# Kernel tuning notes

Measured on AMD Instinct MI355X. Metric: run time of the kernel, lower is better.

## Reference

```python
import jax, jax.numpy as jnp
import numpy as np

OBS_LEN = 16          # observation_len in SnapKV
KERNEL = 5            # AvgPool1d kernel_size
MAX_CACHE_LEN = 2048  # max_cache_length


def _avg_pool1d_nopad(x, k=KERNEL):
    """AvgPool1d(kernel=k, stride=1, padding=k//2, count_include_pad=False) over last axis."""
    S = x.shape[-1]
    pad = k // 2
    zero = jnp.zeros(x.shape[:-1] + (1,), x.dtype)
    c0 = jnp.concatenate([zero, jnp.cumsum(x, axis=-1)], axis=-1)  # [..., S+1]
    i = jnp.arange(S)
    hi = jnp.minimum(i + pad + 1, S)  # exclusive window end
    lo = jnp.maximum(i - pad, 0)      # inclusive window start
    wsum = jnp.take(c0, hi, axis=-1) - jnp.take(c0, lo, axis=-1)
    return wsum / (hi - lo).astype(x.dtype)


def setup_inputs() -> dict:
    key = jax.random.key(0)
    k1, k2, k3 = jax.random.split(key, 3)
    B, H, Q, S, D = 1, 32, 64, 8192, 128
    # realistic attention weights: softmax over key axis
    attn = jax.nn.softmax(jax.random.normal(k1, (B, H, Q, S), jnp.float32), axis=-1)
    k_val = jax.random.normal(k2, (B, H, S, D), jnp.float32)
    v_val = jax.random.normal(k3, (B, H, S, D), jnp.float32)
    input_pos = jnp.arange(S, dtype=jnp.int32)
    return {"attn": attn, "k_val": k_val, "v_val": v_val, "input_pos": input_pos}


def reference(attn, k_val, v_val, input_pos):
    # ---- SnapKV prompt compression (_compress_prompt_w_snapkv) ----
    # priority: mean attention received by each key over the last OBS_LEN queries
    priority = attn[:, :, -OBS_LEN:, :].mean(axis=2)          # [B, H, S]
    attn_history = priority                                    # pre-pooling copy
    pooled = _avg_pool1d_nopad(priority)                       # [B, H, S]
    pooled = pooled.at[:, :, -OBS_LEN:].set(1.0)               # always keep observation window
    _, keep_idxs = jax.lax.top_k(pooled, MAX_CACHE_LEN)        # [B, H, L]
    keep_idxs = jnp.sort(keep_idxs, axis=-1)
    attn_history_c = jnp.take_along_axis(attn_history, keep_idxs, axis=-1)  # [B, H, L]
    idx4 = keep_idxs[..., None]                                # [B, H, L, 1]
    k_compressed = jnp.take_along_axis(k_val, idx4, axis=2)    # [B, H, L, D]
    v_compressed = jnp.take_along_axis(v_val, idx4, axis=2)    # [B, H, L, D]
    # ---- cache fill (update / fill_headwise): compressed tokens fill the whole cache ----
    k_cache = k_compressed
    v_cache = v_compressed
    pos = keep_idxs[0].astype(jnp.int32)                       # head-specific positions, [H, L]
    return k_cache, v_cache, attn_history_c, pos
```

## Files before the change

### kernel.cpp

```cpp
#include <hip/hip_runtime.h>

#define H 32
#define Q 64
#define S 8192
#define D 128
#define OBS 16
#define L 2048

__global__ void k_priority(const float* __restrict__ attn, float* __restrict__ prio) {
    int gid = blockIdx.x;
    int h = gid >> 3;
    int chunk = gid & 7;
    int s4 = chunk * 1024 + threadIdx.x * 4;
    const float4* base = (const float4*)(attn + ((size_t)(h * Q + (Q - OBS)) * S + s4));
    float4 acc = make_float4(0.f, 0.f, 0.f, 0.f);
#pragma unroll
    for (int qq = 0; qq < OBS; ++qq) {
        float4 v = base[qq * (S / 4)];
        acc.x += v.x; acc.y += v.y; acc.z += v.z; acc.w += v.w;
    }
    const float inv = 1.0f / (float)OBS;
    acc.x *= inv; acc.y *= inv; acc.z *= inv; acc.w *= inv;
    *((float4*)(prio + (size_t)h * S + s4)) = acc;
}

__global__ __launch_bounds__(1024) void k_select(const float* __restrict__ prio,
                                                 int* __restrict__ keep,
                                                 float* __restrict__ hist_out,
                                                 float* __restrict__ pos_out) {
    __shared__ float pr[S];
    __shared__ int whist[16][257];
    __shared__ int wtot[16];
    __shared__ int res_byte, res_k;
    const int h = blockIdx.x;
    const int tid = threadIdx.x;
    const int lane = tid & 63, wid = tid >> 6;

    {
        const float4* src = (const float4*)(prio + (size_t)h * S);
        ((float4*)pr)[tid] = src[tid];
        ((float4*)pr)[tid + 1024] = src[tid + 1024];
    }
    __syncthreads();

    unsigned key[8];
    const int s0 = tid * 8;
    {
        float w[12];
#pragma unroll
        for (int i = 0; i < 12; ++i) {
            int idx = s0 - 2 + i;
            w[i] = (idx >= 0 && idx < S) ? pr[idx] : 0.f;
        }
#pragma unroll
        for (int j = 0; j < 8; ++j) {
            int s = s0 + j;
            float pooled;
            if (s >= S - OBS) {
                pooled = 1.0f;
            } else {
                int lo = s - 2; if (lo < 0) lo = 0;
                int hi = s + 3;
                float sum = 0.f;
                for (int i = lo; i < hi; ++i) sum += w[i - s0 + 2];
                pooled = sum / (float)(hi - lo);
            }
            key[j] = __float_as_uint(pooled);
        }
    }

    unsigned prefix = 0;
    int k = L;
    for (int pass = 3; pass >= 0; --pass) {
        for (int i = tid; i < 16 * 257; i += 1024) ((int*)whist)[i] = 0;
        __syncthreads();
        const int shift = pass * 8;
        {
            int cur = -1, run = 0;
#pragma unroll
            for (int j = 0; j < 8; ++j) {
                unsigned kk = key[j];
                bool match = (pass == 3) || ((kk >> (shift + 8)) == prefix);
                int b = match ? (int)((kk >> shift) & 255u) : -1;
                if (b != cur) {
                    if (cur >= 0) atomicAdd(&whist[wid][cur], run);
                    cur = b; run = 1;
                } else {
                    run++;
                }
            }
            if (cur >= 0) atomicAdd(&whist[wid][cur], run);
        }
        __syncthreads();
        if (wid == 0) {
            int b0 = 0, b1 = 0, b2 = 0, b3 = 0;
            const int bb0 = 4 * lane;
#pragma unroll
            for (int w = 0; w < 16; ++w) {
                b0 += whist[w][bb0 + 0];
                b1 += whist[w][bb0 + 1];
                b2 += whist[w][bb0 + 2];
                b3 += whist[w][bb0 + 3];
            }
            int lane_sum = b0 + b1 + b2 + b3;
            int suffix = lane_sum;
#pragma unroll
            for (int off = 1; off < 64; off <<= 1) {
                int u = __shfl_down(suffix, off);
                if (lane + off < 64) suffix += u;
            }
            int suffix_next = suffix - lane_sum;
            if (suffix >= k && suffix_next < k) {
                int bins[4] = {b0, b1, b2, b3};
                int cum = suffix_next;
                for (int bb = 3; bb >= 0; --bb) {
                    int nc = cum + bins[bb];
                    if (nc >= k) { res_byte = bb0 + bb; res_k = k - cum; break; }
                    cum = nc;
                }
            }
        }
        __syncthreads();
        prefix = (prefix << 8) | (unsigned)res_byte;
        k = res_k;
    }
    const unsigned T = prefix;
    const int needed_eq = k;

    int gt = 0, eq = 0;
#pragma unroll
    for (int j = 0; j < 8; ++j) {
        gt += (key[j] > T) ? 1 : 0;
        eq += (key[j] == T) ? 1 : 0;
    }
    int packed = (gt << 16) | eq;
    int v = packed;
#pragma unroll
    for (int off = 1; off < 64; off <<= 1) {
        int u = __shfl_up(v, off);
        if (lane >= off) v += u;
    }
    if (lane == 63) wtot[wid] = v;
    __syncthreads();
    int base = 0;
    for (int w = 0; w < wid; ++w) base += wtot[w];
    int excl = base + v - packed;
    int gt_before = excl >> 16;
    int eq_before = excl & 0xffff;

    {
        int g = gt_before, e = eq_before;
#pragma unroll
        for (int j = 0; j < 8; ++j) {
            bool isgt = key[j] > T;
            bool iseq = key[j] == T;
            bool sel = isgt || (iseq && (e < needed_eq));
            if (sel) {
                int s = s0 + j;
                int rank = g + (e < needed_eq ? e : needed_eq);
                size_t o = (size_t)h * L + rank;
                keep[o] = s;
                pos_out[o] = (float)s;
                hist_out[o] = pr[s];
            }
            g += isgt ? 1 : 0;
            e += iseq ? 1 : 0;
        }
    }
}

__global__ void k_gather(const float* __restrict__ kv_k, const float* __restrict__ kv_v,
                         const int* __restrict__ keep, float* __restrict__ out) {
    const int tid = threadIdx.x;
    const int idx = blockIdx.x * 8 + (tid >> 5);
    const int lane = tid & 31;
    const int h = idx >> 11;
    const int s = keep[idx];
    const float4* srcK = (const float4*)(kv_k + (size_t)(h * S + s) * D);
    const float4* srcV = (const float4*)(kv_v + (size_t)(h * S + s) * D);
    float4* dstK = (float4*)(out + (size_t)idx * D);
    float4* dstV = (float4*)(out + ((size_t)H * L + idx) * D);
    dstK[lane] = srcK[lane];
    dstV[lane] = srcV[lane];
}

extern "C" void kernel_launch(void* const* d_in, const int* in_sizes, int n_in,
                              void* d_out, int out_size, void* d_ws, size_t ws_size,
                              hipStream_t stream) {
    const float* attn = (const float*)d_in[0];
    const float* k_val = (const float*)d_in[1];
    const float* v_val = (const float*)d_in[2];

    float* out = (float*)d_out;
    float* hist = out + (size_t)2 * H * L * D;
    float* pos = hist + (size_t)H * L;

    float* prio = (float*)d_ws;
    int* keep = (int*)((char*)d_ws + (size_t)H * S * sizeof(float));

    k_priority<<<256, 256, 0, stream>>>(attn, prio);
    k_select<<<H, 1024, 0, stream>>>(prio, keep, hist, pos);
    k_gather<<<(H * L) / 8, 256, 0, stream>>>(k_val, v_val, keep, out);
}
```

Measured before the change: 296.9 us.

## Fuse priority, selection and gather into one persistent kernel with flag sync

Merges the three kernels into a single 256-block launch. Every block computes one priority chunk, the first 32 blocks then run the per-head radix select, and all blocks gather K/V rows once their head's selection flag is set. Global-memory counters and flags, reset by a memset, replace the kernel boundaries. This removes launch gaps and lets the gather for finished heads overlap with selection of others, but it relies on all 256 blocks being co-resident (spin-waits could deadlock otherwise) and adds a memset launch.

```diff
diff --git a/kernel.cpp b/kernel.cpp
--- a/kernel.cpp
+++ b/kernel.cpp
@@ -7,181 +7,216 @@
 #define OBS 16
 #define L 2048
 
-__global__ void k_priority(const float* __restrict__ attn, float* __restrict__ prio) {
-    int gid = blockIdx.x;
-    int h = gid >> 3;
-    int chunk = gid & 7;
-    int s4 = chunk * 1024 + threadIdx.x * 4;
-    const float4* base = (const float4*)(attn + ((size_t)(h * Q + (Q - OBS)) * S + s4));
-    float4 acc = make_float4(0.f, 0.f, 0.f, 0.f);
-#pragma unroll
-    for (int qq = 0; qq < OBS; ++qq) {
-        float4 v = base[qq * (S / 4)];
-        acc.x += v.x; acc.y += v.y; acc.z += v.z; acc.w += v.w;
-    }
-    const float inv = 1.0f / (float)OBS;
-    acc.x *= inv; acc.y *= inv; acc.z *= inv; acc.w *= inv;
-    *((float4*)(prio + (size_t)h * S + s4)) = acc;
-}
-
-__global__ __launch_bounds__(1024) void k_select(const float* __restrict__ prio,
-                                                 int* __restrict__ keep,
-                                                 float* __restrict__ hist_out,
-                                                 float* __restrict__ pos_out) {
+__global__ __launch_bounds__(1024) void k_fused(
+    const float* __restrict__ attn,
+    const float* __restrict__ kv_k,
+    const float* __restrict__ kv_v,
+    float* __restrict__ prio,
+    int* __restrict__ keep,
+    int* __restrict__ pdone,
+    int* __restrict__ sflag,
+    float* __restrict__ out,
+    float* __restrict__ hist_out,
+    float* __restrict__ pos_out)
+{
     __shared__ float pr[S];
     __shared__ int whist[16][257];
     __shared__ int wtot[16];
     __shared__ int res_byte, res_k;
-    const int h = blockIdx.x;
+
+    const int bid = blockIdx.x;
     const int tid = threadIdx.x;
     const int lane = tid & 63, wid = tid >> 6;
 
+    if (tid < 256) {
+        const int h = bid >> 3;
+        const int chunk = bid & 7;
+        const int s4 = chunk * 1024 + tid * 4;
+        const float4* base = (const float4*)(attn + ((size_t)(h * Q + (Q - OBS)) * S + s4));
+        float4 acc = make_float4(0.f, 0.f, 0.f, 0.f);
+#pragma unroll
+        for (int qq = 0; qq < OBS; ++qq) {
+            float4 v = base[qq * (S / 4)];
+            acc.x += v.x; acc.y += v.y; acc.z += v.z; acc.w += v.w;
+        }
+        const float inv = 1.0f / (float)OBS;
+        acc.x *= inv; acc.y *= inv; acc.z *= inv; acc.w *= inv;
+        *((float4*)(prio + (size_t)(bid >> 3) * S + s4)) = acc;
+    }
+    __syncthreads();
+    if (tid == 0) {
+        __threadfence();
+        atomicAdd(&pdone[bid >> 3], 1);
+    }
+
+    if (bid < H) {
+        const int h = bid;
+        if (tid == 0) {
+            while (atomicAdd(&pdone[h], 0) < 8) __builtin_amdgcn_s_sleep(2);
+            __threadfence();
+        }
+        __syncthreads();
+
+        {
+            const float4* src = (const float4*)(prio + (size_t)h * S);
+            ((float4*)pr)[tid] = src[tid];
+            ((float4*)pr)[tid + 1024] = src[tid + 1024];
+        }
+        __syncthreads();
+
+        unsigned key[8];
+        const int s0 = tid * 8;
+        {
+            float w[12];
+#pragma unroll
+            for (int i = 0; i < 12; ++i) {
+                int idx = s0 - 2 + i;
+                w[i] = (idx >= 0 && idx < S) ? pr[idx] : 0.f;
+            }
+#pragma unroll
+            for (int j = 0; j < 8; ++j) {
+                int s = s0 + j;
+                float pooled;
+                if (s >= S - OBS) {
+                    pooled = 1.0f;
+                } else {
+                    int lo = s - 2; if (lo < 0) lo = 0;
+                    int hi = s + 3;
+                    float sum = 0.f;
+                    for (int i = lo; i < hi; ++i) sum += w[i - s0 + 2];
+                    pooled = sum / (float)(hi - lo);
+                }
+                key[j] = __float_as_uint(pooled);
+            }
+        }
+
+        unsigned prefix = 0;
+        int k = L;
+        for (int pass = 3; pass >= 0; --pass) {
+            for (int i = tid; i < 16 * 257; i += 1024) ((int*)whist)[i] = 0;
+            __syncthreads();
+            const int shift = pass * 8;
+            {
+                int cur = -1, run = 0;
+#pragma unroll
+                for (int j = 0; j < 8; ++j) {
+                    unsigned kk = key[j];
+                    bool match = (pass == 3) || ((kk >> (shift + 8)) == prefix);
+                    int b = match ? (int)((kk >> shift) & 255u) : -1;
+                    if (b != cur) {
+                        if (cur >= 0) atomicAdd(&whist[wid][cur], run);
+                        cur = b; run = 1;
+                    } else {
+                        run++;
+                    }
+                }
+                if (cur >= 0) atomicAdd(&whist[wid][cur], run);
+            }
+            __syncthreads();
+            if (wid == 0) {
+                int b0 = 0, b1 = 0, b2 = 0, b3 = 0;
+                const int bb0 = 4 * lane;
+#pragma unroll
+                for (int w = 0; w < 16; ++w) {
+                    b0 += whist[w][bb0 + 0];
+                    b1 += whist[w][bb0 + 1];
+                    b2 += whist[w][bb0 + 2];
+                    b3 += whist[w][bb0 + 3];
+                }
+                int lane_sum = b0 + b1 + b2 + b3;
+                int suffix = lane_sum;
+#pragma unroll
+                for (int off = 1; off < 64; off <<= 1) {
+                    int u = __shfl_down(suffix, off);
+                    if (lane + off < 64) suffix += u;
+                }
+                int suffix_next = suffix - lane_sum;
+                if (suffix >= k && suffix_next < k) {
+                    int bins[4] = {b0, b1, b2, b3};
+                    int cum = suffix_next;
+                    for (int bb = 3; bb >= 0; --bb) {
+                        int nc = cum + bins[bb];
+                        if (nc >= k) { res_byte = bb0 + bb; res_k = k - cum; break; }
+                        cum = nc;
+                    }
+                }
+            }
+            __syncthreads();
+            prefix = (prefix << 8) | (unsigned)res_byte;
+            k = res_k;
+        }
+        const unsigned T = prefix;
+        const int needed_eq = k;
+
+        int gt = 0, eq = 0;
+#pragma unroll
+        for (int j = 0; j < 8; ++j) {
+            gt += (key[j] > T) ? 1 : 0;
+            eq += (key[j] == T) ? 1 : 0;
+        }
+        int packed = (gt << 16) | eq;
+        int v = packed;
+#pragma unroll
+        for (int off = 1; off < 64; off <<= 1) {
+            int u = __shfl_up(v, off);
+            if (lane >= off) v += u;
+        }
+        if (lane == 63) wtot[wid] = v;
+        __syncthreads();
+        int base = 0;
+        for (int w = 0; w < wid; ++w) base += wtot[w];
+        int excl = base + v - packed;
+        int gt_before = excl >> 16;
+        int eq_before = excl & 0xffff;
+
+        {
+            int g = gt_before, e = eq_before;
+#pragma unroll
+            for (int j = 0; j < 8; ++j) {
+                bool isgt = key[j] > T;
+                bool iseq = key[j] == T;
+                bool sel = isgt || (iseq && (e < needed_eq));
+                if (sel) {
+                    int s = s0 + j;
+                    int rank = g + (e < needed_eq ? e : needed_eq);
+                    size_t o = (size_t)h * L + rank;
+                    keep[o] = s;
+                    pos_out[o] = (float)s;
+                    hist_out[o] = pr[s];
+                }
+                g += isgt ? 1 : 0;
+                e += iseq ? 1 : 0;
+            }
+        }
+        __syncthreads();
+        if (tid == 0) {
+            __threadfence();
+            atomicExch(&sflag[h], 1);
+        }
+    }
+
     {
-        const float4* src = (const float4*)(prio + (size_t)h * S);
-        ((float4*)pr)[tid] = src[tid];
-        ((float4*)pr)[tid + 1024] = src[tid + 1024];
-    }
-    __syncthreads();
-
-    unsigned key[8];
-    const int s0 = tid * 8;
-    {
-        float w[12];
-#pragma unroll
-        for (int i = 0; i < 12; ++i) {
-            int idx = s0 - 2 + i;
-            w[i] = (idx >= 0 && idx < S) ? pr[idx] : 0.f;
-        }
-#pragma unroll
+        const int h = bid >> 3;
+        if (tid == 0) {
+            while (atomicAdd(&sflag[h], 0) == 0) __builtin_amdgcn_s_sleep(2);
+            __threadfence();
+        }
+        __syncthreads();
+        const int g = (bid << 5) | (tid >> 5);
+        const int l32 = tid & 31;
+        const int r0 = g << 3;
+#pragma unroll 2
         for (int j = 0; j < 8; ++j) {
-            int s = s0 + j;
-            float pooled;
-            if (s >= S - OBS) {
-                pooled = 1.0f;
-            } else {
-                int lo = s - 2; if (lo < 0) lo = 0;
-                int hi = s + 3;
-                float sum = 0.f;
-                for (int i = lo; i < hi; ++i) sum += w[i - s0 + 2];
-                pooled = sum / (float)(hi - lo);
-            }
-            key[j] = __float_as_uint(pooled);
-        }
-    }
-
-    unsigned prefix = 0;
-    int k = L;
-    for (int pass = 3; pass >= 0; --pass) {
-        for (int i = tid; i < 16 * 257; i += 1024) ((int*)whist)[i] = 0;
-        __syncthreads();
-        const int shift = pass * 8;
-        {
-            int cur = -1, run = 0;
-#pragma unroll
-            for (int j = 0; j < 8; ++j) {
-                unsigned kk = key[j];
-                bool match = (pass == 3) || ((kk >> (shift + 8)) == prefix);
-                int b = match ? (int)((kk >> shift) & 255u) : -1;
-                if (b != cur) {
-                    if (cur >= 0) atomicAdd(&whist[wid][cur], run);
-                    cur = b; run = 1;
-                } else {
-                    run++;
-                }
-            }
-            if (cur >= 0) atomicAdd(&whist[wid][cur], run);
-        }
-        __syncthreads();
-        if (wid == 0) {
-            int b0 = 0, b1 = 0, b2 = 0, b3 = 0;
-            const int bb0 = 4 * lane;
-#pragma unroll
-            for (int w = 0; w < 16; ++w) {
-                b0 += whist[w][bb0 + 0];
-                b1 += whist[w][bb0 + 1];
-                b2 += whist[w][bb0 + 2];
-                b3 += whist[w][bb0 + 3];
-            }
-            int lane_sum = b0 + b1 + b2 + b3;
-            int suffix = lane_sum;
-#pragma unroll
-            for (int off = 1; off < 64; off <<= 1) {
-                int u = __shfl_down(suffix, off);
-                if (lane + off < 64) suffix += u;
-            }
-            int suffix_next = suffix - lane_sum;
-            if (suffix >= k && suffix_next < k) {
-                int bins[4] = {b0, b1, b2, b3};
-                int cum = suffix_next;
-                for (int bb = 3; bb >= 0; --bb) {
-                    int nc = cum + bins[bb];
-                    if (nc >= k) { res_byte = bb0 + bb; res_k = k - cum; break; }
-                    cum = nc;
-                }
-            }
-        }
-        __syncthreads();
-        prefix = (prefix << 8) | (unsigned)res_byte;
-        k = res_k;
-    }
-    const unsigned T = prefix;
-    const int needed_eq = k;
-
-    int gt = 0, eq = 0;
-#pragma unroll
-    for (int j = 0; j < 8; ++j) {
-        gt += (key[j] > T) ? 1 : 0;
-        eq += (key[j] == T) ? 1 : 0;
-    }
-    int packed = (gt << 16) | eq;
-    int v = packed;
-#pragma unroll
-    for (int off = 1; off < 64; off <<= 1) {
-        int u = __shfl_up(v, off);
-        if (lane >= off) v += u;
-    }
-    if (lane == 63) wtot[wid] = v;
-    __syncthreads();
-    int base = 0;
-    for (int w = 0; w < wid; ++w) base += wtot[w];
-    int excl = base + v - packed;
-    int gt_before = excl >> 16;
-    int eq_before = excl & 0xffff;
-
-    {
-        int g = gt_before, e = eq_before;
-#pragma unroll
-        for (int j = 0; j < 8; ++j) {
-            bool isgt = key[j] > T;
-            bool iseq = key[j] == T;
-            bool sel = isgt || (iseq && (e < needed_eq));
-            if (sel) {
-                int s = s0 + j;
-                int rank = g + (e < needed_eq ? e : needed_eq);
-                size_t o = (size_t)h * L + rank;
-                keep[o] = s;
-                pos_out[o] = (float)s;
-                hist_out[o] = pr[s];
-            }
-            g += isgt ? 1 : 0;
-            e += iseq ? 1 : 0;
-        }
-    }
-}
-
-__global__ void k_gather(const float* __restrict__ kv_k, const float* __restrict__ kv_v,
-                         const int* __restrict__ keep, float* __restrict__ out) {
-    const int tid = threadIdx.x;
-    const int idx = blockIdx.x * 8 + (tid >> 5);
-    const int lane = tid & 31;
-    const int h = idx >> 11;
-    const int s = keep[idx];
-    const float4* srcK = (const float4*)(kv_k + (size_t)(h * S + s) * D);
-    const float4* srcV = (const float4*)(kv_v + (size_t)(h * S + s) * D);
-    float4* dstK = (float4*)(out + (size_t)idx * D);
-    float4* dstV = (float4*)(out + ((size_t)H * L + idx) * D);
-    dstK[lane] = srcK[lane];
-    dstV[lane] = srcV[lane];
+            const int idx = r0 + j;
+            const int s = keep[idx];
+            const float4* srcK = (const float4*)(kv_k + (size_t)(h * S + s) * D);
+            const float4* srcV = (const float4*)(kv_v + (size_t)(h * S + s) * D);
+            float4* dstK = (float4*)(out + (size_t)idx * D);
+            float4* dstV = (float4*)(out + ((size_t)H * L + idx) * D);
+            dstK[l32] = srcK[l32];
+            dstV[l32] = srcV[l32];
+        }
+    }
 }
 
 extern "C" void kernel_launch(void* const* d_in, const int* in_sizes, int n_in,
@@ -195,10 +230,12 @@
     float* hist = out + (size_t)2 * H * L * D;
     float* pos = hist + (size_t)H * L;
 
-    float* prio = (float*)d_ws;
-    int* keep = (int*)((char*)d_ws + (size_t)H * S * sizeof(float));
-
-    k_priority<<<256, 256, 0, stream>>>(attn, prio);
-    k_select<<<H, 1024, 0, stream>>>(prio, keep, hist, pos);
-    k_gather<<<(H * L) / 8, 256, 0, stream>>>(k_val, v_val, keep, out);
+    int* pdone = (int*)d_ws;
+    int* sflag = pdone + 32;
+    float* prio = (float*)((char*)d_ws + 256);
+    int* keep = (int*)((char*)d_ws + 256 + (size_t)H * S * sizeof(float));
+
+    hipMemsetAsync(d_ws, 0, 256, stream);
+    k_fused<<<256, 1024, 0, stream>>>(attn, k_val, v_val, prio, keep, pdone, sflag,
+                                      out, hist, pos);
 }
```

New measurement: 318.9 us. 7.4% more time.

## Fuse top-k selection and KV gather into one kernel with per-head flags

Applied to the files above, without the earlier changes.

Merges the selection and gather kernels into a single 256-block launch. The first 32 blocks each run the radix-select for one head and then raise a per-head release flag. Every block then spin-waits on the flag for its head and gathers 256 rows of K and V, so gathering one head can overlap selection of the others. The per-pass histogram clears and their barriers are removed by giving each pass its own histogram slice. The spin-wait relies on the 32 selection blocks being co-resident, and each 1024-thread block holds 32 KB plus about 66 KB of LDS, so a waiting block can occupy a CU while it does nothing.

```diff
diff --git a/kernel.cpp b/kernel.cpp
--- a/kernel.cpp
+++ b/kernel.cpp
@@ -7,7 +7,9 @@
 #define OBS 16
 #define L 2048
 
-__global__ void k_priority(const float* __restrict__ attn, float* __restrict__ prio) {
+__global__ void k_priority(const float* __restrict__ attn, float* __restrict__ prio,
+                           int* __restrict__ sflag) {
+    if (blockIdx.x == 0 && threadIdx.x < H) sflag[threadIdx.x * 32] = 0;
     int gid = blockIdx.x;
     int h = gid >> 3;
     int chunk = gid & 7;
@@ -24,164 +26,193 @@
     *((float4*)(prio + (size_t)h * S + s4)) = acc;
 }
 
-__global__ __launch_bounds__(1024) void k_select(const float* __restrict__ prio,
-                                                 int* __restrict__ keep,
-                                                 float* __restrict__ hist_out,
-                                                 float* __restrict__ pos_out) {
+__global__ __launch_bounds__(1024) void k_selgather(
+    const float* __restrict__ prio,
+    const float* __restrict__ kv_k,
+    const float* __restrict__ kv_v,
+    int* __restrict__ keep,
+    int* __restrict__ sflag,
+    float* __restrict__ out,
+    float* __restrict__ hist_out,
+    float* __restrict__ pos_out)
+{
     __shared__ float pr[S];
-    __shared__ int whist[16][257];
+    __shared__ int whist[4][16][257];
     __shared__ int wtot[16];
     __shared__ int res_byte, res_k;
-    const int h = blockIdx.x;
+
+    const int bid = blockIdx.x;
     const int tid = threadIdx.x;
     const int lane = tid & 63, wid = tid >> 6;
 
+    if (bid < H) {
+        const int h = bid;
+
+        {
+            const float4* src = (const float4*)(prio + (size_t)h * S);
+            ((float4*)pr)[tid] = src[tid];
+            ((float4*)pr)[tid + 1024] = src[tid + 1024];
+            for (int i = tid; i < 4 * 16 * 257; i += 1024) ((int*)whist)[i] = 0;
+        }
+        __syncthreads();
+
+        unsigned key[8];
+        const int s0 = tid * 8;
+        {
+            float w[12];
+#pragma unroll
+            for (int i = 0; i < 12; ++i) {
+                int idx = s0 - 2 + i;
+                w[i] = (idx >= 0 && idx < S) ? pr[idx] : 0.f;
+            }
+#pragma unroll
+            for (int j = 0; j < 8; ++j) {
+                int s = s0 + j;
+                float pooled;
+                if (s >= S - OBS) {
+                    pooled = 1.0f;
+                } else {
+                    int lo = s - 2; if (lo < 0) lo = 0;
+                    int hi = s + 3;
+                    float sum = 0.f;
+                    for (int i = lo; i < hi; ++i) sum += w[i - s0 + 2];
+                    pooled = sum / (float)(hi - lo);
+                }
+                key[j] = __float_as_uint(pooled);
+            }
+        }
+
+        unsigned prefix = 0;
+        int k = L;
+        for (int pass = 3; pass >= 0; --pass) {
+            const int shift = pass * 8;
+            {
+                int cur = -1, run = 0;
+#pragma unroll
+                for (int j = 0; j < 8; ++j) {
+                    unsigned kk = key[j];
+                    bool match = (pass == 3) || ((kk >> (shift + 8)) == prefix);
+                    int b = match ? (int)((kk >> shift) & 255u) : -1;
+                    if (b != cur) {
+                        if (cur >= 0) atomicAdd(&whist[pass][wid][cur], run);
+                        cur = b; run = 1;
+                    } else {
+                        run++;
+                    }
+                }
+                if (cur >= 0) atomicAdd(&whist[pass][wid][cur], run);
+            }
+            __syncthreads();
+            if (wid == 0) {
+                int b0 = 0, b1 = 0, b2 = 0, b3 = 0;
+                const int bb0 = 4 * lane;
+#pragma unroll
+                for (int w = 0; w < 16; ++w) {
+                    b0 += whist[pass][w][bb0 + 0];
+                    b1 += whist[pass][w][bb0 + 1];
+                    b2 += whist[pass][w][bb0 + 2];
+                    b3 += whist[pass][w][bb0 + 3];
+                }
+                int lane_sum = b0 + b1 + b2 + b3;
+                int suffix = lane_sum;
+#pragma unroll
+                for (int off = 1; off < 64; off <<= 1) {
+                    int u = __shfl_down(suffix, off);
+                    if (lane + off < 64) suffix += u;
+                }
+                int suffix_next = suffix - lane_sum;
+                if (suffix >= k && suffix_next < k) {
+                    int bins[4] = {b0, b1, b2, b3};
+                    int cum = suffix_next;
+                    for (int bb = 3; bb >= 0; --bb) {
+                        int nc = cum + bins[bb];
+                        if (nc >= k) { res_byte = bb0 + bb; res_k = k - cum; break; }
+                        cum = nc;
+                    }
+                }
+            }
+            __syncthreads();
+            prefix = (prefix << 8) | (unsigned)res_byte;
+            k = res_k;
+        }
+        const unsigned T = prefix;
+        const int needed_eq = k;
+
+        int gt = 0, eq = 0;
+#pragma unroll
+        for (int j = 0; j < 8; ++j) {
+            gt += (key[j] > T) ? 1 : 0;
+            eq += (key[j] == T) ? 1 : 0;
+        }
+        int packed = (gt << 16) | eq;
+        int v = packed;
+#pragma unroll
+        for (int off = 1; off < 64; off <<= 1) {
+            int u = __shfl_up(v, off);
+            if (lane >= off) v += u;
+        }
+        if (lane == 63) wtot[wid] = v;
+        __syncthreads();
+        int base = 0;
+        for (int w = 0; w < wid; ++w) base += wtot[w];
+        int excl = base + v - packed;
+        int gt_before = excl >> 16;
+        int eq_before = excl & 0xffff;
+
+        {
+            int g = gt_before, e = eq_before;
+#pragma unroll
+            for (int j = 0; j < 8; ++j) {
+                bool isgt = key[j] > T;
+                bool iseq = key[j] == T;
+                bool sel = isgt || (iseq && (e < needed_eq));
+                if (sel) {
+                    int s = s0 + j;
+                    int rank = g + (e < needed_eq ? e : needed_eq);
+                    size_t o = (size_t)h * L + rank;
+                    keep[o] = s;
+                    pos_out[o] = (float)s;
+                    hist_out[o] = pr[s];
+                }
+                g += isgt ? 1 : 0;
+                e += iseq ? 1 : 0;
+            }
+        }
+        __syncthreads();
+        if (tid == 0) {
+            __threadfence();
+            __hip_atomic_store(&sflag[h * 32], 1, __ATOMIC_RELEASE,
+                               __HIP_MEMORY_SCOPE_AGENT);
+        }
+    }
+
     {
-        const float4* src = (const float4*)(prio + (size_t)h * S);
-        ((float4*)pr)[tid] = src[tid];
-        ((float4*)pr)[tid + 1024] = src[tid + 1024];
+        const int gh = bid >> 3;
+        if (tid == 0) {
+            while (__hip_atomic_load(&sflag[gh * 32], __ATOMIC_ACQUIRE,
+                                     __HIP_MEMORY_SCOPE_AGENT) == 0)
+                __builtin_amdgcn_s_sleep(8);
+            __threadfence();
+        }
+        __syncthreads();
+
+        const int r0 = ((bid << 5) | (tid >> 5)) << 3;
+        const int l32 = tid & 31;
+#pragma unroll
+        for (int jj = 0; jj < 8; jj += 4) {
+            int sI[4];
+#pragma unroll
+            for (int t = 0; t < 4; ++t) sI[t] = keep[r0 + jj + t];
+#pragma unroll
+            for (int t = 0; t < 4; ++t) {
+                const int idx = r0 + jj + t;
+                const float4* srcK = (const float4*)(kv_k + (size_t)(gh * S + sI[t]) * D);
+                const float4* srcV = (const float4*)(kv_v + (size_t)(gh * S + sI[t]) * D);
+                ((float4*)(out + (size_t)idx * D))[l32] = srcK[l32];
+                ((float4*)(out + ((size_t)H * L + idx) * D))[l32] = srcV[l32];
+            }
+        }
     }
-    __syncthreads();
-
-    unsigned key[8];
-    const int s0 = tid * 8;
-    {
-        float w[12];
-#pragma unroll
-        for (int i = 0; i < 12; ++i) {
-            int idx = s0 - 2 + i;
-            w[i] = (idx >= 0 && idx < S) ? pr[idx] : 0.f;
-        }
-#pragma unroll
-        for (int j = 0; j < 8; ++j) {
-            int s = s0 + j;
-            float pooled;
-            if (s >= S - OBS) {
-                pooled = 1.0f;
-            } else {
-                int lo = s - 2; if (lo < 0) lo = 0;
-                int hi = s + 3;
-                float sum = 0.f;
-                for (int i = lo; i < hi; ++i) sum += w[i - s0 + 2];
-                pooled = sum / (float)(hi - lo);
-            }
-            key[j] = __float_as_uint(pooled);
-        }
-    }
-
-    unsigned prefix = 0;
-    int k = L;
-    for (int pass = 3; pass >= 0; --pass) {
-        for (int i = tid; i < 16 * 257; i += 1024) ((int*)whist)[i] = 0;
-        __syncthreads();
-        const int shift = pass * 8;
-        {
-            int cur = -1, run = 0;
-#pragma unroll
-            for (int j = 0; j < 8; ++j) {
-                unsigned kk = key[j];
-                bool match = (pass == 3) || ((kk >> (shift + 8)) == prefix);
-                int b = match ? (int)((kk >> shift) & 255u) : -1;
-                if (b != cur) {
-                    if (cur >= 0) atomicAdd(&whist[wid][cur], run);
-                    cur = b; run = 1;
-                } else {
-                    run++;
-                }
-            }
-            if (cur >= 0) atomicAdd(&whist[wid][cur], run);
-        }
-        __syncthreads();
-        if (wid == 0) {
-            int b0 = 0, b1 = 0, b2 = 0, b3 = 0;
-            const int bb0 = 4 * lane;
-#pragma unroll
-            for (int w = 0; w < 16; ++w) {
-                b0 += whist[w][bb0 + 0];
-                b1 += whist[w][bb0 + 1];
-                b2 += whist[w][bb0 + 2];
-                b3 += whist[w][bb0 + 3];
-            }
-            int lane_sum = b0 + b1 + b2 + b3;
-            int suffix = lane_sum;
-#pragma unroll
-            for (int off = 1; off < 64; off <<= 1) {
-                int u = __shfl_down(suffix, off);
-                if (lane + off < 64) suffix += u;
-            }
-            int suffix_next = suffix - lane_sum;
-            if (suffix >= k && suffix_next < k) {
-                int bins[4] = {b0, b1, b2, b3};
-                int cum = suffix_next;
-                for (int bb = 3; bb >= 0; --bb) {
-                    int nc = cum + bins[bb];
-                    if (nc >= k) { res_byte = bb0 + bb; res_k = k - cum; break; }
-                    cum = nc;
-                }
-            }
-        }
-        __syncthreads();
-        prefix = (prefix << 8) | (unsigned)res_byte;
-        k = res_k;
-    }
-    const unsigned T = prefix;
-    const int needed_eq = k;
-
-    int gt = 0, eq = 0;
-#pragma unroll
-    for (int j = 0; j < 8; ++j) {
-        gt += (key[j] > T) ? 1 : 0;
-        eq += (key[j] == T) ? 1 : 0;
-    }
-    int packed = (gt << 16) | eq;
-    int v = packed;
-#pragma unroll
-    for (int off = 1; off < 64; off <<= 1) {
-        int u = __shfl_up(v, off);
-        if (lane >= off) v += u;
-    }
-    if (lane == 63) wtot[wid] = v;
-    __syncthreads();
-    int base = 0;
-    for (int w = 0; w < wid; ++w) base += wtot[w];
-    int excl = base + v - packed;
-    int gt_before = excl >> 16;
-    int eq_before = excl & 0xffff;
-
-    {
-        int g = gt_before, e = eq_before;
-#pragma unroll
-        for (int j = 0; j < 8; ++j) {
-            bool isgt = key[j] > T;
-            bool iseq = key[j] == T;
-            bool sel = isgt || (iseq && (e < needed_eq));
-            if (sel) {
-                int s = s0 + j;
-                int rank = g + (e < needed_eq ? e : needed_eq);
-                size_t o = (size_t)h * L + rank;
-                keep[o] = s;
-                pos_out[o] = (float)s;
-                hist_out[o] = pr[s];
-            }
-            g += isgt ? 1 : 0;
-            e += iseq ? 1 : 0;
-        }
-    }
-}
-
-__global__ void k_gather(const float* __restrict__ kv_k, const float* __restrict__ kv_v,
-                         const int* __restrict__ keep, float* __restrict__ out) {
-    const int tid = threadIdx.x;
-    const int idx = blockIdx.x * 8 + (tid >> 5);
-    const int lane = tid & 31;
-    const int h = idx >> 11;
-    const int s = keep[idx];
-    const float4* srcK = (const float4*)(kv_k + (size_t)(h * S + s) * D);
-    const float4* srcV = (const float4*)(kv_v + (size_t)(h * S + s) * D);
-    float4* dstK = (float4*)(out + (size_t)idx * D);
-    float4* dstV = (float4*)(out + ((size_t)H * L + idx) * D);
-    dstK[lane] = srcK[lane];
-    dstV[lane] = srcV[lane];
 }
 
 extern "C" void kernel_launch(void* const* d_in, const int* in_sizes, int n_in,
@@ -195,10 +226,11 @@
     float* hist = out + (size_t)2 * H * L * D;
     float* pos = hist + (size_t)H * L;
 
-    float* prio = (float*)d_ws;
-    int* keep = (int*)((char*)d_ws + (size_t)H * S * sizeof(float));
-
-    k_priority<<<256, 256, 0, stream>>>(attn, prio);
-    k_select<<<H, 1024, 0, stream>>>(prio, keep, hist, pos);
-    k_gather<<<(H * L) / 8, 256, 0, stream>>>(k_val, v_val, keep, out);
+    int* sflag = (int*)d_ws;
+    float* prio = (float*)((char*)d_ws + 4096);
+    int* keep = (int*)((char*)d_ws + 4096 + (size_t)H * S * sizeof(float));
+
+    k_priority<<<256, 256, 0, stream>>>(attn, prio, sflag);
+    k_selgather<<<256, 1024, 0, stream>>>(prio, k_val, v_val, keep, sflag,
+                                          out, hist, pos);
 }
```

After: 318.4 us. 7.2% more time.

## Fuse priority reduction into top-k select kernel and widen gather per warp

Applied to the files above, without the earlier changes.

Merges the priority mean computation into the selection kernel, so each head's block reads the last 16 attention rows directly and the workspace round trip and one launch go away. Histogram buffers are now allocated per pass and cleared once up front, which removes a barrier per radix pass. The gather kernel handles four rows per half-wavefront with a vector load of the indices and uses nontemporal loads and stores. The cost is that the fused kernel runs on only 32 blocks, so the attention read gets far less parallelism than the 256-block priority kernel it replaces.

```diff
diff --git a/kernel.cpp b/kernel.cpp
--- a/kernel.cpp
+++ b/kernel.cpp
@@ -7,39 +7,37 @@
 #define OBS 16
 #define L 2048
 
-__global__ void k_priority(const float* __restrict__ attn, float* __restrict__ prio) {
-    int gid = blockIdx.x;
-    int h = gid >> 3;
-    int chunk = gid & 7;
-    int s4 = chunk * 1024 + threadIdx.x * 4;
-    const float4* base = (const float4*)(attn + ((size_t)(h * Q + (Q - OBS)) * S + s4));
-    float4 acc = make_float4(0.f, 0.f, 0.f, 0.f);
-#pragma unroll
-    for (int qq = 0; qq < OBS; ++qq) {
-        float4 v = base[qq * (S / 4)];
-        acc.x += v.x; acc.y += v.y; acc.z += v.z; acc.w += v.w;
-    }
-    const float inv = 1.0f / (float)OBS;
-    acc.x *= inv; acc.y *= inv; acc.z *= inv; acc.w *= inv;
-    *((float4*)(prio + (size_t)h * S + s4)) = acc;
-}
-
-__global__ __launch_bounds__(1024) void k_select(const float* __restrict__ prio,
-                                                 int* __restrict__ keep,
-                                                 float* __restrict__ hist_out,
-                                                 float* __restrict__ pos_out) {
+typedef float f32x4 __attribute__((ext_vector_type(4)));
+
+__global__ __launch_bounds__(1024) void k_priosel(
+    const float* __restrict__ attn,
+    int* __restrict__ keep,
+    float* __restrict__ hist_out,
+    float* __restrict__ pos_out)
+{
     __shared__ float pr[S];
-    __shared__ int whist[16][257];
+    __shared__ int whist[4][16][257];
     __shared__ int wtot[16];
     __shared__ int res_byte, res_k;
+
     const int h = blockIdx.x;
     const int tid = threadIdx.x;
     const int lane = tid & 63, wid = tid >> 6;
 
+    for (int i = tid; i < 4 * 16 * 257; i += 1024) ((int*)whist)[i] = 0;
+
     {
-        const float4* src = (const float4*)(prio + (size_t)h * S);
-        ((float4*)pr)[tid] = src[tid];
-        ((float4*)pr)[tid + 1024] = src[tid + 1024];
+        const float* abase = attn + (size_t)(h * Q + (Q - OBS)) * S;
+        f32x4 a0 = {0.f, 0.f, 0.f, 0.f}, a1 = a0;
+#pragma unroll
+        for (int q = 0; q < OBS; ++q) {
+            const f32x4* row = (const f32x4*)(abase + (size_t)q * S);
+            a0 += __builtin_nontemporal_load(row + tid);
+            a1 += __builtin_nontemporal_load(row + tid + 1024);
+        }
+        const float inv = 1.0f / (float)OBS;
+        ((f32x4*)pr)[tid] = a0 * inv;
+        ((f32x4*)pr)[tid + 1024] = a1 * inv;
     }
     __syncthreads();
 
@@ -72,8 +70,6 @@
     unsigned prefix = 0;
     int k = L;
     for (int pass = 3; pass >= 0; --pass) {
-        for (int i = tid; i < 16 * 257; i += 1024) ((int*)whist)[i] = 0;
-        __syncthreads();
         const int shift = pass * 8;
         {
             int cur = -1, run = 0;
@@ -83,13 +79,13 @@
                 bool match = (pass == 3) || ((kk >> (shift + 8)) == prefix);
                 int b = match ? (int)((kk >> shift) & 255u) : -1;
                 if (b != cur) {
-                    if (cur >= 0) atomicAdd(&whist[wid][cur], run);
+                    if (cur >= 0) atomicAdd(&whist[pass][wid][cur], run);
                     cur = b; run = 1;
                 } else {
                     run++;
                 }
             }
-            if (cur >= 0) atomicAdd(&whist[wid][cur], run);
+            if (cur >= 0) atomicAdd(&whist[pass][wid][cur], run);
         }
         __syncthreads();
         if (wid == 0) {
@@ -97,10 +93,10 @@
             const int bb0 = 4 * lane;
 #pragma unroll
             for (int w = 0; w < 16; ++w) {
-                b0 += whist[w][bb0 + 0];
-                b1 += whist[w][bb0 + 1];
-                b2 += whist[w][bb0 + 2];
-                b3 += whist[w][bb0 + 3];
+                b0 += whist[pass][w][bb0 + 0];
+                b1 += whist[pass][w][bb0 + 1];
+                b2 += whist[pass][w][bb0 + 2];
+                b3 += whist[pass][w][bb0 + 3];
             }
             int lane_sum = b0 + b1 + b2 + b3;
             int suffix = lane_sum;
@@ -172,16 +168,21 @@
 __global__ void k_gather(const float* __restrict__ kv_k, const float* __restrict__ kv_v,
                          const int* __restrict__ keep, float* __restrict__ out) {
     const int tid = threadIdx.x;
-    const int idx = blockIdx.x * 8 + (tid >> 5);
-    const int lane = tid & 31;
-    const int h = idx >> 11;
-    const int s = keep[idx];
-    const float4* srcK = (const float4*)(kv_k + (size_t)(h * S + s) * D);
-    const float4* srcV = (const float4*)(kv_v + (size_t)(h * S + s) * D);
-    float4* dstK = (float4*)(out + (size_t)idx * D);
-    float4* dstV = (float4*)(out + ((size_t)H * L + idx) * D);
-    dstK[lane] = srcK[lane];
-    dstV[lane] = srcV[lane];
+    const int l32 = tid & 31;
+    const int i0 = (blockIdx.x * 8 + (tid >> 5)) * 4;
+    const int h = i0 >> 11;
+    const int4 kk = *(const int4*)(keep + i0);
+    const int sI[4] = {kk.x, kk.y, kk.z, kk.w};
+#pragma unroll
+    for (int t = 0; t < 4; ++t) {
+        const int idx = i0 + t;
+        const f32x4* srcK = (const f32x4*)(kv_k + (size_t)(h * S + sI[t]) * D);
+        const f32x4* srcV = (const f32x4*)(kv_v + (size_t)(h * S + sI[t]) * D);
+        f32x4* dstK = (f32x4*)(out + (size_t)idx * D);
+        f32x4* dstV = (f32x4*)(out + ((size_t)H * L + idx) * D);
+        __builtin_nontemporal_store(__builtin_nontemporal_load(srcK + l32), dstK + l32);
+        __builtin_nontemporal_store(__builtin_nontemporal_load(srcV + l32), dstV + l32);
+    }
 }
 
 extern "C" void kernel_launch(void* const* d_in, const int* in_sizes, int n_in,
@@ -195,10 +196,8 @@
     float* hist = out + (size_t)2 * H * L * D;
     float* pos = hist + (size_t)H * L;
 
-    float* prio = (float*)d_ws;
-    int* keep = (int*)((char*)d_ws + (size_t)H * S * sizeof(float));
-
-    k_priority<<<256, 256, 0, stream>>>(attn, prio);
-    k_select<<<H, 1024, 0, stream>>>(prio, keep, hist, pos);
-    k_gather<<<(H * L) / 8, 256, 0, stream>>>(k_val, v_val, keep, out);
+    int* keep = (int*)d_ws;
+
+    k_priosel<<<H, 1024, 0, stream>>>(attn, keep, hist, pos);
+    k_gather<<<(H * L) / 32, 256, 0, stream>>>(k_val, v_val, keep, out);
 }
```

Measured after the change: 288.4 us. -2.9%, faster.
